# Optimization experiments

Measured on AMD Instinct MI355X. Metric: run time of the kernel, lower is better.

Reference implementation:

```python
import jax, jax.numpy as jnp
import numpy as np

B, T, IMG, PS, D, DEPTH, NH = 1, 8, 224, 16, 768, 12, 12
HP = IMG // PS
NP = HP * HP          # 196 patches per frame
N = NP + 1            # +1 cls token per frame
DH = D // NH
MLP = 4 * D
SCALE = DH ** -0.5


def _ln(x, g, b):
    mu = x.mean(-1, keepdims=True)
    var = ((x - mu) ** 2).mean(-1, keepdims=True)
    return (x - mu) / jnp.sqrt(var + 1e-5) * g + b


def _forward(x, W_patch, b_patch, cls_token, pos_embed,
             ln1_g, ln1_b, qkv_w, qkv_b, proj_w, proj_b,
             ln2_g, ln2_b, fc1_w, fc1_b, fc2_w, fc2_b, lnf_g, lnf_b):
    Bc = x.shape[0]
    # --- patch embed (Conv3d k=(1,ps,ps), stride=(1,ps,ps) == per-frame patch matmul) ---
    p = x.reshape(Bc, T, 3, HP, PS, HP, PS).transpose(0, 1, 3, 5, 2, 4, 6)
    p = p.reshape(Bc, T, NP, 3 * PS * PS)
    emb = p @ W_patch.T + b_patch                     # [B,T,NP,D] (correct layout)
    # replicate torch flatten(3)/transpose(1,2)/reshape axis scramble:
    emb = jnp.swapaxes(emb, 2, 3).reshape(Bc, T, NP, D)
    cls = jnp.broadcast_to(cls_token.reshape(1, 1, 1, D), (Bc, T, 1, D))
    h = jnp.concatenate([cls, emb], axis=2) + pos_embed.reshape(1, 1, N, D)
    h = h.reshape(Bc, T * N, D)

    for i in range(DEPTH):
        # --- attention ---
        a = _ln(h, ln1_g[i], ln1_b[i])
        qkv = (a @ qkv_w[i] + qkv_b[i]).reshape(Bc, T * N, 3, NH, DH)
        q, k, v = (jnp.transpose(qkv[:, :, j], (0, 2, 1, 3)) for j in range(3))  # [B,H,S,dh]
        if i % 2 == 0:  # divided space-time
            qf = q.reshape(Bc, NH, T, N, DH)
            kf = k.reshape(Bc, NH, T, N, DH)
            vf = v.reshape(Bc, NH, T, N, DH)
            q_t = qf.mean(3, keepdims=True)           # [B,H,T,1,dh]
            k_t = kf.mean(3, keepdims=True)
            v_t = vf.mean(3, keepdims=True)
            attn_t = jax.nn.softmax(jnp.einsum('bhtqd,bhtkd->bhtqk', q_t, k_t) * SCALE, -1)
            x_t = jnp.einsum('bhtqk,bhtkd->bhtqd', attn_t, v_t)[:, :, :, 0]  # [B,H,T,dh]
            attn_s = jax.nn.softmax(jnp.einsum('bhtqd,bhtkd->bhtqk', qf, kf) * SCALE, -1)
            x_s = jnp.einsum('bhtqk,bhtkd->bhtqd', attn_s, vf)               # [B,H,T,N,dh]
            o = (x_s + x_t[:, :, :, None, :]).reshape(Bc, NH, T * N, DH)
        else:  # joint space-time
            attn = jax.nn.softmax(jnp.einsum('bhqd,bhkd->bhqk', q, k) * SCALE, -1)
            o = jnp.einsum('bhqk,bhkd->bhqd', attn, v)
        o = jnp.transpose(o, (0, 2, 1, 3)).reshape(Bc, T * N, D)
        h = h + (o @ proj_w[i] + proj_b[i])
        # --- mlp ---
        m = _ln(h, ln2_g[i], ln2_b[i])
        m = jax.nn.gelu(m @ fc1_w[i] + fc1_b[i], approximate=False)
        h = h + (m @ fc2_w[i] + fc2_b[i])

    return _ln(h, lnf_g, lnf_b).reshape(Bc, T, N, D)


def setup_inputs() -> dict:
    key = jax.random.key(0)
    ks = jax.random.split(key, 12)
    s = 0.02
    return {
        'x': jax.random.normal(ks[0], (B, T, 3, IMG, IMG), jnp.float32),
        'W_patch': jax.random.normal(ks[1], (D, 3 * PS * PS), jnp.float32) * s,
        'b_patch': jnp.zeros((D,), jnp.float32),
        'cls_token': jax.random.normal(ks[2], (1, 1, D), jnp.float32) * s,
        'pos_embed': jax.random.normal(ks[3], (1, N, D), jnp.float32) * s,
        'ln1_g': jnp.ones((DEPTH, D), jnp.float32),
        'ln1_b': jnp.zeros((DEPTH, D), jnp.float32),
        'qkv_w': jax.random.normal(ks[4], (DEPTH, D, 3 * D), jnp.float32) * s,
        'qkv_b': jnp.zeros((DEPTH, 3 * D), jnp.float32),
        'proj_w': jax.random.normal(ks[5], (DEPTH, D, D), jnp.float32) * s,
        'proj_b': jnp.zeros((DEPTH, D), jnp.float32),
        'ln2_g': jnp.ones((DEPTH, D), jnp.float32),
        'ln2_b': jnp.zeros((DEPTH, D), jnp.float32),
        'fc1_w': jax.random.normal(ks[6], (DEPTH, D, MLP), jnp.float32) * s,
        'fc1_b': jnp.zeros((DEPTH, MLP), jnp.float32),
        'fc2_w': jax.random.normal(ks[7], (DEPTH, MLP, D), jnp.float32) * s,
        'fc2_b': jnp.zeros((DEPTH, D), jnp.float32),
        'lnf_g': jnp.ones((D,), jnp.float32),
        'lnf_b': jnp.zeros((D,), jnp.float32),
    }


def reference(x, W_patch, b_patch, cls_token, pos_embed,
              ln1_g, ln1_b, qkv_w, qkv_b, proj_w, proj_b,
              ln2_g, ln2_b, fc1_w, fc1_b, fc2_w, fc2_b, lnf_g, lnf_b):
    return _forward(x, W_patch, b_patch, cls_token, pos_embed,
                    ln1_g, ln1_b, qkv_w, qkv_b, proj_w, proj_b,
                    ln2_g, ln2_b, fc1_w, fc1_b, fc2_w, fc2_b, lnf_g, lnf_b)
```

## Files before the change

### kernel.cpp

```cpp
#include <hip/hip_runtime.h>
#include <math.h>

#define Dm 768
#define Tn 8
#define Nn 197
#define Sn 1576
#define MLPn 3072
#define NPn 196
#define MPAD 1664

typedef unsigned short u16;
typedef __bf16 bf16x8 __attribute__((ext_vector_type(8)));
typedef float f32x4 __attribute__((ext_vector_type(4)));
typedef unsigned int u32x4 __attribute__((ext_vector_type(4)));
typedef u16 u16x8 __attribute__((ext_vector_type(8)));
typedef u16 u16x4 __attribute__((ext_vector_type(4)));

__device__ inline u16 f2bf(float f) {
    union { float f; unsigned u; } v; v.f = f;
    unsigned r = v.u + 0x7fffu + ((v.u >> 16) & 1u);
    return (u16)(r >> 16);
}
__device__ inline float bf2f(u16 v) {
    union { unsigned u; float f; } x; x.u = ((unsigned)v) << 16; return x.f;
}

__device__ __forceinline__ void gl_lds16(const u16* __restrict__ g, u16* l) {
    __builtin_amdgcn_global_load_lds((const __attribute__((address_space(1))) void*)g,
                                     (__attribute__((address_space(3))) void*)l,
                                     16, 0, 0);
}

__global__ __launch_bounds__(256) void im2col_k(const float* __restrict__ x, u16* __restrict__ P) {
    int idx = blockIdx.x * 256 + threadIdx.x;
    if (idx >= 1568 * 768) return;
    int c = idx % 768, r = idx / 768;
    int p = r % 196, t = r / 196;
    int hp = p / 14, wp = p % 14;
    int ch = c / 256, rem = c % 256, py = rem / 16, px = rem % 16;
    P[idx] = f2bf(x[((t * 3 + ch) * 224 + hp * 16 + py) * 224 + wp * 16 + px]);
}

__global__ __launch_bounds__(256) void cvt_k(const float* __restrict__ s, u16* __restrict__ d, int n) {
    int i = blockIdx.x * 256 + threadIdx.x;
    if (i < n) d[i] = f2bf(s[i]);
}

__global__ __launch_bounds__(256) void cvtT_layer_k(const float* __restrict__ qw, const float* __restrict__ pw,
                                                    const float* __restrict__ f1w, const float* __restrict__ f2w,
                                                    u16* __restrict__ Wq, u16* __restrict__ Wp,
                                                    u16* __restrict__ W1, u16* __restrict__ W2) {
    __shared__ float tile[32][33];
    int bid = blockIdx.x;
    const float* src; u16* dst; int K, N, k0, n0;
    if (bid < 1728)      { src = qw;  dst = Wq; K = 768;  N = 2304; int r = bid;        k0 = (r / 72) * 32; n0 = (r % 72) * 32; }
    else if (bid < 2304) { src = pw;  dst = Wp; K = 768;  N = 768;  int r = bid - 1728; k0 = (r / 24) * 32; n0 = (r % 24) * 32; }
    else if (bid < 4608) { src = f1w; dst = W1; K = 768;  N = 3072; int r = bid - 2304; k0 = (r / 96) * 32; n0 = (r % 96) * 32; }
    else                 { src = f2w; dst = W2; K = 3072; N = 768;  int r = bid - 4608; k0 = (r / 24) * 32; n0 = (r % 24) * 32; }
    int tx = threadIdx.x & 31, ty = threadIdx.x >> 5;
#pragma unroll
    for (int i = 0; i < 4; ++i) tile[ty + 8 * i][tx] = src[(size_t)(k0 + ty + 8 * i) * N + n0 + tx];
    __syncthreads();
#pragma unroll
    for (int i = 0; i < 4; ++i) dst[(size_t)(n0 + ty + 8 * i) * K + k0 + tx] = f2bf(tile[tx][ty + 8 * i]);
}

__global__ __launch_bounds__(256) void build_h_k(const float* __restrict__ emb, const float* __restrict__ cls,
                                                 const float* __restrict__ pos, float* __restrict__ h) {
    int idx = blockIdx.x * 256 + threadIdx.x;
    if (idx >= Sn * Dm) return;
    int d = idx % Dm, s = idx / Dm;
    int t = s / Nn, r = s % Nn;
    float v;
    if (r == 0) v = cls[d];
    else {
        int f = (r - 1) * Dm + d;
        int p = f % NPn, dd = f / NPn;
        v = emb[(size_t)(t * NPn + p) * Dm + dd];
    }
    h[idx] = v + pos[r * Dm + d];
}

template <typename OutT>
__global__ __launch_bounds__(256) void ln_k(const float* __restrict__ X, const float* __restrict__ g,
                                            const float* __restrict__ bta, OutT* __restrict__ Y) {
    int row = blockIdx.x;
    const float* x = X + (size_t)row * Dm;
    float s = 0.f, s2 = 0.f;
#pragma unroll
    for (int q = 0; q < 3; ++q) {
        float v = x[threadIdx.x + q * 256];
        s += v; s2 += v * v;
    }
#pragma unroll
    for (int off = 1; off < 64; off <<= 1) {
        s  += __shfl_xor(s,  off);
        s2 += __shfl_xor(s2, off);
    }
    __shared__ float red[8];
    int wv = threadIdx.x >> 6;
    if ((threadIdx.x & 63) == 0) { red[wv * 2] = s; red[wv * 2 + 1] = s2; }
    __syncthreads();
    s  = red[0] + red[2] + red[4] + red[6];
    s2 = red[1] + red[3] + red[5] + red[7];
    float mu  = s * (1.f / 768.f);
    float var = s2 * (1.f / 768.f) - mu * mu;
    float rstd = rsqrtf(var + 1e-5f);
#pragma unroll
    for (int q = 0; q < 3; ++q) {
        int i = threadIdx.x + q * 256;
        float v = (x[i] - mu) * rstd * g[i] + bta[i];
        if constexpr (sizeof(OutT) == 2) Y[(size_t)row * Dm + i] = f2bf(v);
        else                             Y[(size_t)row * Dm + i] = v;
    }
}

__global__ __launch_bounds__(256) void mgemm_k(const u16* __restrict__ A, const u16* __restrict__ Bt,
                                               float* __restrict__ Cp, int N, int Kfull, int Kc) {
    __shared__ __align__(16) u16 As[4096];
    __shared__ __align__(16) u16 Bs[4096];
    int split = blockIdx.z;
    A  += split * Kc;
    Bt += split * Kc;
    Cp += (size_t)split * MPAD * N;
    int tid = threadIdx.x;
    int lane = tid & 63, w = tid >> 6;
    int wm = w & 1, wn = w >> 1;
    int m0 = blockIdx.y * 128, n0 = blockIdx.x * 128;
    f32x4 acc[4][4] = {};
    int c0 = tid, c1 = tid + 256;
    int ar0 = ((c0 >> 6) << 4) + (c0 & 15), ac0 = ((c0 >> 4) & 3) << 3;
    int ar1 = ((c1 >> 6) << 4) + (c1 & 15), ac1 = ((c1 >> 4) & 3) << 3;
    const u16* Arow0 = A  + (size_t)(m0 + ar0) * Kfull + ac0;
    const u16* Arow1 = A  + (size_t)(m0 + ar1) * Kfull + ac1;
    const u16* Brow0 = Bt + (size_t)(n0 + ar0) * Kfull + ac0;
    const u16* Brow1 = Bt + (size_t)(n0 + ar1) * Kfull + ac1;
    u16* As0 = As + (w * 64) * 8;
    u16* As1 = As + (256 + w * 64) * 8;
    u16* Bs0 = Bs + (w * 64) * 8;
    u16* Bs1 = Bs + (256 + w * 64) * 8;
    for (int k0 = 0; k0 < Kc; k0 += 32) {
        gl_lds16(Arow0 + k0, As0);
        gl_lds16(Arow1 + k0, As1);
        gl_lds16(Brow0 + k0, Bs0);
        gl_lds16(Brow1 + k0, Bs1);
        __syncthreads();
        bf16x8 af[4], bfr[4];
#pragma unroll
        for (int i = 0; i < 4; ++i) {
            af[i]  = *(const bf16x8*)(As + (((wm * 4 + i) * 64 + lane) << 3));
            bfr[i] = *(const bf16x8*)(Bs + (((wn * 4 + i) * 64 + lane) << 3));
        }
#pragma unroll
        for (int mi = 0; mi < 4; ++mi)
#pragma unroll
            for (int ni = 0; ni < 4; ++ni)
                acc[mi][ni] = __builtin_amdgcn_mfma_f32_16x16x32_bf16(af[mi], bfr[ni], acc[mi][ni], 0, 0, 0);
        __syncthreads();
    }
    int rbase = (lane >> 4) << 2, cl = lane & 15;
#pragma unroll
    for (int mi = 0; mi < 4; ++mi)
#pragma unroll
        for (int r = 0; r < 4; ++r) {
            int gm = m0 + wm * 64 + mi * 16 + rbase + r;
#pragma unroll
            for (int ni = 0; ni < 4; ++ni) {
                int gn = n0 + wn * 64 + ni * 16 + cl;
                Cp[(size_t)gm * N + gn] = acc[mi][ni][r];
            }
        }
}

template <bool GELU_ACT>
__global__ __launch_bounds__(256) void mgemm_fused_k(const u16* __restrict__ A, const u16* __restrict__ Bt,
                                                     const float* __restrict__ bias, u16* __restrict__ out,
                                                     int N, int Kfull, int Mout) {
    __shared__ __align__(16) u16 As[64 * 32];
    __shared__ __align__(16) u16 Bs[128 * 32];
    int tid = threadIdx.x;
    int lane = tid & 63, w = tid >> 6;
    int wm = w & 1, wn = w >> 1;
    int m0 = blockIdx.y * 64, n0 = blockIdx.x * 128;
    f32x4 acc[2][4] = {};
    int ca = tid;
    int ar = ((ca >> 6) << 4) + (ca & 15), ac = ((ca >> 4) & 3) << 3;
    const u16* Arow = A + (size_t)(m0 + ar) * Kfull + ac;
    int cb1 = tid + 256;
    int br1 = ((cb1 >> 6) << 4) + (cb1 & 15), bc1 = ((cb1 >> 4) & 3) << 3;
    const u16* Brow0 = Bt + (size_t)(n0 + ar) * Kfull + ac;
    const u16* Brow1 = Bt + (size_t)(n0 + br1) * Kfull + bc1;
    u16* Asw  = As + (w * 64) * 8;
    u16* Bsw0 = Bs + (w * 64) * 8;
    u16* Bsw1 = Bs + (256 + w * 64) * 8;
    for (int k0 = 0; k0 < Kfull; k0 += 32) {
        gl_lds16(Arow + k0, Asw);
        gl_lds16(Brow0 + k0, Bsw0);
        gl_lds16(Brow1 + k0, Bsw1);
        __syncthreads();
        bf16x8 af[2], bfr[4];
#pragma unroll
        for (int i = 0; i < 2; ++i) af[i]  = *(const bf16x8*)(As + (((wm * 2 + i) * 64 + lane) << 3));
#pragma unroll
        for (int j = 0; j < 4; ++j) bfr[j] = *(const bf16x8*)(Bs + (((wn * 4 + j) * 64 + lane) << 3));
#pragma unroll
        for (int mi = 0; mi < 2; ++mi)
#pragma unroll
            for (int ni = 0; ni < 4; ++ni)
                acc[mi][ni] = __builtin_amdgcn_mfma_f32_16x16x32_bf16(af[mi], bfr[ni], acc[mi][ni], 0, 0, 0);
        __syncthreads();
    }
    int rbase = (lane >> 4) << 2, cl = lane & 15;
#pragma unroll
    for (int mi = 0; mi < 2; ++mi)
#pragma unroll
        for (int r = 0; r < 4; ++r) {
            int gm = m0 + wm * 32 + mi * 16 + rbase + r;
            if (gm < Mout) {
#pragma unroll
                for (int ni = 0; ni < 4; ++ni) {
                    int gn = n0 + wn * 64 + ni * 16 + cl;
                    float v = acc[mi][ni][r] + bias[gn];
                    if (GELU_ACT) v = 0.5f * v * (1.f + erff(v * 0.7071067811865476f));
                    out[(size_t)gm * N + gn] = f2bf(v);
                }
            }
        }
}

__global__ __launch_bounds__(256) void ep_k(const float* __restrict__ Cp, const float* __restrict__ bias,
                                            float* __restrict__ out, int N, int S) {
    int row = blockIdx.y;
    int n = blockIdx.x * 1024 + threadIdx.x * 4;
    if (n >= N) return;
    size_t off = (size_t)row * N + n;
    f32x4 acc = *(const f32x4*)(Cp + off);
    for (int s = 1; s < S; ++s)
        acc += *(const f32x4*)(Cp + (size_t)s * MPAD * N + off);
    acc += *(const f32x4*)(bias + n);
    *(f32x4*)(out + off) = acc;
}

template <bool FINALOUT>
__global__ __launch_bounds__(256) void ep_ln_k(const float* __restrict__ Cp, const float* __restrict__ bias,
                                               float* __restrict__ h, const float* __restrict__ g,
                                               const float* __restrict__ bta, void* __restrict__ lnout, int S) {
    int row = blockIdx.x;
    int t = threadIdx.x;
    float v[3];
    float s = 0.f, s2 = 0.f;
#pragma unroll
    for (int q = 0; q < 3; ++q) {
        int i = t + q * 256;
        size_t off = (size_t)row * Dm + i;
        float a = Cp[off];
        for (int sp = 1; sp < S; ++sp) a += Cp[(size_t)sp * MPAD * Dm + off];
        a += bias[i] + h[off];
        h[off] = a;
        v[q] = a; s += a; s2 += a * a;
    }
#pragma unroll
    for (int off = 1; off < 64; off <<= 1) {
        s  += __shfl_xor(s,  off);
        s2 += __shfl_xor(s2, off);
    }
    __shared__ float red[8];
    int wv = t >> 6;
    if ((t & 63) == 0) { red[wv * 2] = s; red[wv * 2 + 1] = s2; }
    __syncthreads();
    s  = red[0] + red[2] + red[4] + red[6];
    s2 = red[1] + red[3] + red[5] + red[7];
    float mu  = s * (1.f / 768.f);
    float var = s2 * (1.f / 768.f) - mu * mu;
    float rstd = rsqrtf(var + 1e-5f);
#pragma unroll
    for (int q = 0; q < 3; ++q) {
        int i = t + q * 256;
        float y = (v[q] - mu) * rstd * g[i] + bta[i];
        if constexpr (FINALOUT) ((float*)lnout)[(size_t)row * Dm + i] = y;
        else                    ((u16*)lnout)[(size_t)row * Dm + i] = f2bf(y);
    }
}

__global__ __launch_bounds__(64) void vmean_k(const u16* __restrict__ qkv, float* __restrict__ vm) {
    int g = blockIdx.x;
    int h = g >> 3, t = g & 7;
    int d = threadIdx.x;
    float s = 0.f;
    for (int n = 0; n < Nn; ++n)
        s += bf2f(qkv[(size_t)(t * Nn + n) * 2304 + 1536 + h * 64 + d]);
    vm[g * 64 + d] = s * (1.f / 197.f);
}

__global__ __launch_bounds__(256) void attn_mfma_k(const u16* __restrict__ qkv, float* __restrict__ Ou,
                                                   float* __restrict__ ml, int even, int nsplit,
                                                   int NG, int Sq) {
    __shared__ __align__(16) u16 Ks[64 * 64];
    __shared__ __align__(16) u16 Vt[64 * 64];
    __shared__ __align__(16) u16 Ps[4 * 32 * 64];
    int g = blockIdx.y;
    int h, sbase;
    if (even) { h = g >> 3; sbase = (g & 7) * Nn; } else { h = g; sbase = 0; }
    int split = blockIdx.z;
    int chunk = (Sq + nsplit - 1) / nsplit;
    int kbeg = split * chunk, kend = min(Sq, kbeg + chunk);
    int tid = threadIdx.x, lane = tid & 63, w = tid >> 6;
    int quad = lane >> 4, l15 = lane & 15;
    int q0w = blockIdx.x * 128 + w * 32;
    u16* Pw = Ps + w * 2048;

    bf16x8 aq[2][2];
#pragma unroll
    for (int mb = 0; mb < 2; ++mb) {
        int qidx = q0w + mb * 16 + l15; if (qidx >= Sq) qidx = Sq - 1;
        const u16* qp = qkv + (size_t)(sbase + qidx) * 2304 + h * 64;
#pragma unroll
        for (int ks = 0; ks < 2; ++ks)
            aq[mb][ks] = *(const bf16x8*)(qp + ks * 32 + quad * 8);
    }
    f32x4 acc_o[2][4] = {};
    float m_run[2][4], l_run[2][4];
#pragma unroll
    for (int mb = 0; mb < 2; ++mb)
#pragma unroll
        for (int r = 0; r < 4; ++r) { m_run[mb][r] = -INFINITY; l_run[mb][r] = 0.f; }

    for (int kt = kbeg; kt < kend; kt += 64) {
        int cnt = kend - kt; if (cnt > 64) cnt = 64;
        {
            int dc = tid & 7;
#pragma unroll
            for (int p = 0; p < 2; ++p) {
                int row = (tid >> 3) + 32 * p;
                u32x4 kd = {};
                if (row < cnt) kd = *(const u32x4*)(qkv + (size_t)(sbase + kt + row) * 2304 + 768 + h * 64 + dc * 8);
                *(u32x4*)(Ks + row * 64 + ((dc ^ (row & 7)) << 3)) = kd;
            }
        }
        {
            int d = (tid & 31) * 2, kc = tid >> 5;
            u16x8 lo, hi;
#pragma unroll
            for (int i = 0; i < 8; ++i) {
                int key = kc * 8 + i;
                unsigned t = 0;
                if (key < cnt) t = *(const unsigned*)(qkv + (size_t)(sbase + kt + key) * 2304 + 1536 + h * 64 + d);
                lo[i] = (u16)(t & 0xffffu); hi[i] = (u16)(t >> 16);
            }
            *(u16x8*)(Vt + d * 64 + ((kc ^ (d & 7)) << 3)) = lo;
            *(u16x8*)(Vt + (d + 1) * 64 + ((kc ^ ((d + 1) & 7)) << 3)) = hi;
        }
        __syncthreads();
        f32x4 acc_s[2][4] = {};
#pragma unroll
        for (int ni = 0; ni < 4; ++ni) {
            int key = l15 + ni * 16;
#pragma unroll
            for (int ks = 0; ks < 2; ++ks) {
                bf16x8 bk = *(const bf16x8*)(Ks + key * 64 + ((((ks << 2) + quad) ^ (key & 7)) << 3));
                acc_s[0][ni] = __builtin_amdgcn_mfma_f32_16x16x32_bf16(aq[0][ks], bk, acc_s[0][ni], 0, 0, 0);
                acc_s[1][ni] = __builtin_amdgcn_mfma_f32_16x16x32_bf16(aq[1][ks], bk, acc_s[1][ni], 0, 0, 0);
            }
        }
#pragma unroll
        for (int mb = 0; mb < 2; ++mb) {
#pragma unroll
            for (int ni = 0; ni < 4; ++ni) {
                int keyabs = kt + l15 + ni * 16;
#pragma unroll
                for (int r = 0; r < 4; ++r) {
                    float sv = acc_s[mb][ni][r] * 0.125f;
                    if (keyabs >= kend) sv = -1e30f;
                    acc_s[mb][ni][r] = sv;
                }
            }
#pragma unroll
            for (int r = 0; r < 4; ++r) {
                float mx = fmaxf(fmaxf(acc_s[mb][0][r], acc_s[mb][1][r]), fmaxf(acc_s[mb][2][r], acc_s[mb][3][r]));
                mx = fmaxf(mx, __shfl_xor(mx, 1));
                mx = fmaxf(mx, __shfl_xor(mx, 2));
                mx = fmaxf(mx, __shfl_xor(mx, 4));
                mx = fmaxf(mx, __shfl_xor(mx, 8));
                float mnew = fmaxf(m_run[mb][r], mx);
                float pv[4], ps = 0.f;
#pragma unroll
                for (int ni = 0; ni < 4; ++ni) { pv[ni] = __expf(acc_s[mb][ni][r] - mnew); ps += pv[ni]; }
                ps += __shfl_xor(ps, 1);
                ps += __shfl_xor(ps, 2);
                ps += __shfl_xor(ps, 4);
                ps += __shfl_xor(ps, 8);
                float alpha = __expf(m_run[mb][r] - mnew);
                l_run[mb][r] = l_run[mb][r] * alpha + ps;
                m_run[mb][r] = mnew;
#pragma unroll
                for (int ni = 0; ni < 4; ++ni) acc_o[mb][ni][r] *= alpha;
                int prow = mb * 16 + quad * 4 + r;
#pragma unroll
                for (int ni = 0; ni < 4; ++ni) {
                    int key = l15 + ni * 16;
                    Pw[prow * 64 + (((key >> 3) ^ (prow & 7)) << 3) + (key & 7)] = f2bf(pv[ni]);
                }
            }
        }
        bf16x8 ap[2][2];
#pragma unroll
        for (int mb = 0; mb < 2; ++mb)
#pragma unroll
            for (int ks = 0; ks < 2; ++ks)
                ap[mb][ks] = *(const bf16x8*)(Pw + (mb * 16 + l15) * 64 + ((((ks << 2) + quad) ^ (l15 & 7)) << 3));
#pragma unroll
        for (int ni = 0; ni < 4; ++ni) {
            int d = l15 + ni * 16;
#pragma unroll
            for (int ks = 0; ks < 2; ++ks) {
                bf16x8 bv = *(const bf16x8*)(Vt + d * 64 + ((((ks << 2) + quad) ^ (d & 7)) << 3));
                acc_o[0][ni] = __builtin_amdgcn_mfma_f32_16x16x32_bf16(ap[0][ks], bv, acc_o[0][ni], 0, 0, 0);
                acc_o[1][ni] = __builtin_amdgcn_mfma_f32_16x16x32_bf16(ap[1][ks], bv, acc_o[1][ni], 0, 0, 0);
            }
        }
        __syncthreads();
    }
    size_t gb = ((size_t)split * NG + g) * Sq;
#pragma unroll
    for (int mb = 0; mb < 2; ++mb)
#pragma unroll
        for (int r = 0; r < 4; ++r) {
            int q = q0w + mb * 16 + quad * 4 + r;
            if (q < Sq) {
                float* op = Ou + (gb + q) * 64;
#pragma unroll
                for (int ni = 0; ni < 4; ++ni) op[l15 + ni * 16] = acc_o[mb][ni][r];
                if (l15 == 0) {
                    ml[(gb + q) * 2]     = m_run[mb][r];
                    ml[(gb + q) * 2 + 1] = l_run[mb][r];
                }
            }
        }
}

__global__ __launch_bounds__(256) void comb_k(const float* __restrict__ Ou, const float* __restrict__ ml,
                                              const float* __restrict__ vm, u16* __restrict__ ob,
                                              int even, int nsplit, int NG, int Sq) {
    int g = blockIdx.y;
    int q = blockIdx.x * 4 + (threadIdx.x >> 6);
    int d = threadIdx.x & 63;
    if (q >= Sq) return;
    int h, sbase;
    if (even) { h = g >> 3; sbase = (g & 7) * Nn; } else { h = g; sbase = 0; }
    float M = -INFINITY;
    for (int s = 0; s < nsplit; ++s) M = fmaxf(M, ml[(((size_t)s * NG + g) * Sq + q) * 2]);
    float num = 0.f, den = 0.f;
    for (int s = 0; s < nsplit; ++s) {
        size_t base = ((size_t)s * NG + g) * Sq + q;
        float wgt = __expf(ml[base * 2] - M);
        den += wgt * ml[base * 2 + 1];
        num += wgt * Ou[base * 64 + d];
    }
    float o = num / den;
    if (even) o += vm[g * 64 + d];
    ob[(size_t)(sbase + q) * Dm + h * 64 + d] = f2bf(o);
}

extern "C" void kernel_launch(void* const* d_in, const int* in_sizes, int n_in,
                              void* d_out, int out_size, void* d_ws, size_t ws_size,
                              hipStream_t stream) {
    (void)in_sizes; (void)n_in; (void)out_size; (void)ws_size;
    const float* x       = (const float*)d_in[0];
    const float* W_patch = (const float*)d_in[1];
    const float* b_patch = (const float*)d_in[2];
    const float* cls     = (const float*)d_in[3];
    const float* pos     = (const float*)d_in[4];
    const float* ln1_g   = (const float*)d_in[5];
    const float* ln1_b   = (const float*)d_in[6];
    const float* qkv_w   = (const float*)d_in[7];
    const float* qkv_b   = (const float*)d_in[8];
    const float* proj_w  = (const float*)d_in[9];
    const float* proj_b  = (const float*)d_in[10];
    const float* ln2_g   = (const float*)d_in[11];
    const float* ln2_b   = (const float*)d_in[12];
    const float* fc1_w   = (const float*)d_in[13];
    const float* fc1_b   = (const float*)d_in[14];
    const float* fc2_w   = (const float*)d_in[15];
    const float* fc2_b   = (const float*)d_in[16];
    const float* lnf_g   = (const float*)d_in[17];
    const float* lnf_b   = (const float*)d_in[18];

    char* base = (char*)d_ws;
    auto alloc = [&](size_t bytes) { void* p = base; base += (bytes + 255) & ~(size_t)255; return p; };
    u16*   P    = (u16*)  alloc((size_t)MPAD * 768 * 2);
    u16*   Wq   = (u16*)  alloc((size_t)2304 * 768 * 2);
    u16*   Wp   = (u16*)  alloc((size_t)768 * 768 * 2);
    u16*   W1   = (u16*)  alloc((size_t)3072 * 768 * 2);
    u16*   W2   = (u16*)  alloc((size_t)768 * 3072 * 2);
    float* emb  = (float*)alloc((size_t)1568 * 768 * 4);
    float* h    = (float*)alloc((size_t)Sn * Dm * 4);
    u16*   a    = (u16*)  alloc((size_t)MPAD * 768 * 2);
    u16*   qkvb = (u16*)  alloc((size_t)Sn * 2304 * 2);
    u16*   ob   = (u16*)  alloc((size_t)MPAD * 768 * 2);
    u16*   mb   = (u16*)  alloc((size_t)MPAD * 3072 * 2);
    float* vm   = (float*)alloc((size_t)96 * 64 * 4);
    float* Ou   = (float*)alloc((size_t)3 * 12 * Sn * 64 * 4);
    float* ml   = (float*)alloc((size_t)3 * 12 * Sn * 2 * 4);
    float* Cp   = (float*)alloc((size_t)4 * MPAD * 768 * 4);

    im2col_k<<<(1568 * 768 + 255) / 256, 256, 0, stream>>>(x, P);
    cvt_k<<<(768 * 768 + 255) / 256, 256, 0, stream>>>(W_patch, Wp, 768 * 768);
    mgemm_k<<<dim3(6, 13, 3), 256, 0, stream>>>(P, Wp, Cp, 768, 768, 256);
    ep_k<<<dim3(1, 1568), 256, 0, stream>>>(Cp, b_patch, emb, 768, 3);
    build_h_k<<<(Sn * Dm + 255) / 256, 256, 0, stream>>>(emb, cls, pos, h);
    ln_k<u16><<<Sn, 256, 0, stream>>>(h, ln1_g, ln1_b, a);

    for (int i = 0; i < 12; ++i) {
        cvtT_layer_k<<<6912, 256, 0, stream>>>(
            qkv_w + (size_t)i * 768 * 2304, proj_w + (size_t)i * 768 * 768,
            fc1_w + (size_t)i * 768 * 3072, fc2_w + (size_t)i * 3072 * 768,
            Wq, Wp, W1, W2);
        mgemm_fused_k<false><<<dim3(18, 26), 256, 0, stream>>>(a, Wq, qkv_b + i * 2304, qkvb, 2304, 768, Sn);
        if ((i & 1) == 0) {
            vmean_k<<<96, 64, 0, stream>>>(qkvb, vm);
            attn_mfma_k<<<dim3(2, 96, 1), 256, 0, stream>>>(qkvb, Ou, ml, 1, 1, 96, Nn);
            comb_k<<<dim3(50, 96), 256, 0, stream>>>(Ou, ml, vm, ob, 1, 1, 96, Nn);
        } else {
            attn_mfma_k<<<dim3(13, 12, 3), 256, 0, stream>>>(qkvb, Ou, ml, 0, 3, 12, Sn);
            comb_k<<<dim3(394, 12), 256, 0, stream>>>(Ou, ml, vm, ob, 0, 3, 12, Sn);
        }
        mgemm_k<<<dim3(6, 13, 4), 256, 0, stream>>>(ob, Wp, Cp, 768, 768, 192);
        ep_ln_k<false><<<Sn, 256, 0, stream>>>(Cp, proj_b + i * Dm, h, ln2_g + i * Dm, ln2_b + i * Dm, a, 4);
        mgemm_fused_k<true><<<dim3(24, 26), 256, 0, stream>>>(a, W1, fc1_b + i * MLPn, mb, 3072, 768, Sn);
        mgemm_k<<<dim3(6, 13, 4), 256, 0, stream>>>(mb, W2, Cp, 768, 3072, 768);
        if (i < 11)
            ep_ln_k<false><<<Sn, 256, 0, stream>>>(Cp, fc2_b + i * Dm, h, ln1_g + (i + 1) * Dm, ln1_b + (i + 1) * Dm, a, 4);
        else
            ep_ln_k<true><<<Sn, 256, 0, stream>>>(Cp, fc2_b + i * Dm, h, lnf_g, lnf_b, d_out, 4);
    }
}
```

Measured before the change: 2.369 ms.

## Double-buffer GEMM LDS tiles, fuse divided-attention normalization, parallelize v-mean

Both MFMA GEMM kernels now double-buffer their LDS tiles, issuing the global-to-LDS loads for the next K step before computing on the current one, with one barrier per iteration instead of two. For divided (even) layers the attention kernel normalizes its output and adds the temporal v-mean itself, so the combine kernel launch and the Ou/ml round trip are dropped. vmean_k uses 256 threads with a shared-memory reduction instead of 64. LDS use per GEMM block doubles, which may lower occupancy.

```diff
diff --git a/kernel.cpp b/kernel.cpp
--- a/kernel.cpp
+++ b/kernel.cpp
@@ -117,8 +117,8 @@
 
 __global__ __launch_bounds__(256) void mgemm_k(const u16* __restrict__ A, const u16* __restrict__ Bt,
                                                float* __restrict__ Cp, int N, int Kfull, int Kc) {
-    __shared__ __align__(16) u16 As[4096];
-    __shared__ __align__(16) u16 Bs[4096];
+    __shared__ __align__(16) u16 As[2 * 4096];
+    __shared__ __align__(16) u16 Bs[2 * 4096];
     int split = blockIdx.z;
     A  += split * Kc;
     Bt += split * Kc;
@@ -135,28 +135,35 @@
     const u16* Arow1 = A  + (size_t)(m0 + ar1) * Kfull + ac1;
     const u16* Brow0 = Bt + (size_t)(n0 + ar0) * Kfull + ac0;
     const u16* Brow1 = Bt + (size_t)(n0 + ar1) * Kfull + ac1;
-    u16* As0 = As + (w * 64) * 8;
-    u16* As1 = As + (256 + w * 64) * 8;
-    u16* Bs0 = Bs + (w * 64) * 8;
-    u16* Bs1 = Bs + (256 + w * 64) * 8;
+    auto STAGE = [&](int buf, int k0) {
+        int bo = buf << 12;
+        gl_lds16(Arow0 + k0, As + bo + (w * 64) * 8);
+        gl_lds16(Arow1 + k0, As + bo + (256 + w * 64) * 8);
+        gl_lds16(Brow0 + k0, Bs + bo + (w * 64) * 8);
+        gl_lds16(Brow1 + k0, Bs + bo + (256 + w * 64) * 8);
+    };
+    STAGE(0, 0);
+    asm volatile("s_waitcnt vmcnt(0)" ::: "memory");
+    __builtin_amdgcn_s_barrier();
+    int cur = 0;
     for (int k0 = 0; k0 < Kc; k0 += 32) {
-        gl_lds16(Arow0 + k0, As0);
-        gl_lds16(Arow1 + k0, As1);
-        gl_lds16(Brow0 + k0, Bs0);
-        gl_lds16(Brow1 + k0, Bs1);
-        __syncthreads();
+        if (k0 + 32 < Kc) STAGE(cur ^ 1, k0 + 32);
+        const u16* Ab = As + (cur << 12);
+        const u16* Bb = Bs + (cur << 12);
         bf16x8 af[4], bfr[4];
 #pragma unroll
         for (int i = 0; i < 4; ++i) {
-            af[i]  = *(const bf16x8*)(As + (((wm * 4 + i) * 64 + lane) << 3));
-            bfr[i] = *(const bf16x8*)(Bs + (((wn * 4 + i) * 64 + lane) << 3));
+            af[i]  = *(const bf16x8*)(Ab + (((wm * 4 + i) * 64 + lane) << 3));
+            bfr[i] = *(const bf16x8*)(Bb + (((wn * 4 + i) * 64 + lane) << 3));
         }
 #pragma unroll
         for (int mi = 0; mi < 4; ++mi)
 #pragma unroll
             for (int ni = 0; ni < 4; ++ni)
                 acc[mi][ni] = __builtin_amdgcn_mfma_f32_16x16x32_bf16(af[mi], bfr[ni], acc[mi][ni], 0, 0, 0);
-        __syncthreads();
+        asm volatile("s_waitcnt vmcnt(0)" ::: "memory");
+        __builtin_amdgcn_s_barrier();
+        cur ^= 1;
     }
     int rbase = (lane >> 4) << 2, cl = lane & 15;
 #pragma unroll
@@ -176,8 +183,8 @@
 __global__ __launch_bounds__(256) void mgemm_fused_k(const u16* __restrict__ A, const u16* __restrict__ Bt,
                                                      const float* __restrict__ bias, u16* __restrict__ out,
                                                      int N, int Kfull, int Mout) {
-    __shared__ __align__(16) u16 As[64 * 32];
-    __shared__ __align__(16) u16 Bs[128 * 32];
+    __shared__ __align__(16) u16 As[2 * 64 * 32];
+    __shared__ __align__(16) u16 Bs[2 * 128 * 32];
     int tid = threadIdx.x;
     int lane = tid & 63, w = tid >> 6;
     int wm = w & 1, wn = w >> 1;
@@ -190,25 +197,32 @@
     int br1 = ((cb1 >> 6) << 4) + (cb1 & 15), bc1 = ((cb1 >> 4) & 3) << 3;
     const u16* Brow0 = Bt + (size_t)(n0 + ar) * Kfull + ac;
     const u16* Brow1 = Bt + (size_t)(n0 + br1) * Kfull + bc1;
-    u16* Asw  = As + (w * 64) * 8;
-    u16* Bsw0 = Bs + (w * 64) * 8;
-    u16* Bsw1 = Bs + (256 + w * 64) * 8;
+    auto STAGE = [&](int buf, int k0) {
+        gl_lds16(Arow + k0, As + (buf << 11) + (w * 64) * 8);
+        gl_lds16(Brow0 + k0, Bs + (buf << 12) + (w * 64) * 8);
+        gl_lds16(Brow1 + k0, Bs + (buf << 12) + (256 + w * 64) * 8);
+    };
+    STAGE(0, 0);
+    asm volatile("s_waitcnt vmcnt(0)" ::: "memory");
+    __builtin_amdgcn_s_barrier();
+    int cur = 0;
     for (int k0 = 0; k0 < Kfull; k0 += 32) {
-        gl_lds16(Arow + k0, Asw);
-        gl_lds16(Brow0 + k0, Bsw0);
-        gl_lds16(Brow1 + k0, Bsw1);
-        __syncthreads();
+        if (k0 + 32 < Kfull) STAGE(cur ^ 1, k0 + 32);
+        const u16* Ab = As + (cur << 11);
+        const u16* Bb = Bs + (cur << 12);
         bf16x8 af[2], bfr[4];
 #pragma unroll
-        for (int i = 0; i < 2; ++i) af[i]  = *(const bf16x8*)(As + (((wm * 2 + i) * 64 + lane) << 3));
-#pragma unroll
-        for (int j = 0; j < 4; ++j) bfr[j] = *(const bf16x8*)(Bs + (((wn * 4 + j) * 64 + lane) << 3));
+        for (int i = 0; i < 2; ++i) af[i]  = *(const bf16x8*)(Ab + (((wm * 2 + i) * 64 + lane) << 3));
+#pragma unroll
+        for (int j = 0; j < 4; ++j) bfr[j] = *(const bf16x8*)(Bb + (((wn * 4 + j) * 64 + lane) << 3));
 #pragma unroll
         for (int mi = 0; mi < 2; ++mi)
 #pragma unroll
             for (int ni = 0; ni < 4; ++ni)
                 acc[mi][ni] = __builtin_amdgcn_mfma_f32_16x16x32_bf16(af[mi], bfr[ni], acc[mi][ni], 0, 0, 0);
-        __syncthreads();
+        asm volatile("s_waitcnt vmcnt(0)" ::: "memory");
+        __builtin_amdgcn_s_barrier();
+        cur ^= 1;
     }
     int rbase = (lane >> 4) << 2, cl = lane & 15;
 #pragma unroll
@@ -282,19 +296,23 @@
     }
 }
 
-__global__ __launch_bounds__(64) void vmean_k(const u16* __restrict__ qkv, float* __restrict__ vm) {
+__global__ __launch_bounds__(256) void vmean_k(const u16* __restrict__ qkv, float* __restrict__ vm) {
     int g = blockIdx.x;
     int h = g >> 3, t = g & 7;
-    int d = threadIdx.x;
+    int d = threadIdx.x & 63, part = threadIdx.x >> 6;
     float s = 0.f;
-    for (int n = 0; n < Nn; ++n)
+    for (int n = part; n < Nn; n += 4)
         s += bf2f(qkv[(size_t)(t * Nn + n) * 2304 + 1536 + h * 64 + d]);
-    vm[g * 64 + d] = s * (1.f / 197.f);
+    __shared__ float red[256];
+    red[threadIdx.x] = s;
+    __syncthreads();
+    if (part == 0) vm[g * 64 + d] = (red[d] + red[64 + d] + red[128 + d] + red[192 + d]) * (1.f / 197.f);
 }
 
 __global__ __launch_bounds__(256) void attn_mfma_k(const u16* __restrict__ qkv, float* __restrict__ Ou,
-                                                   float* __restrict__ ml, int even, int nsplit,
-                                                   int NG, int Sq) {
+                                                   float* __restrict__ ml, const float* __restrict__ vm,
+                                                   u16* __restrict__ ob, int even, int nsplit,
+                                                   int NG, int Sq, int fuse) {
     __shared__ __align__(16) u16 Ks[64 * 64];
     __shared__ __align__(16) u16 Vt[64 * 64];
     __shared__ __align__(16) u16 Ps[4 * 32 * 64];
@@ -420,33 +438,49 @@
         }
         __syncthreads();
     }
-    size_t gb = ((size_t)split * NG + g) * Sq;
-#pragma unroll
-    for (int mb = 0; mb < 2; ++mb)
-#pragma unroll
-        for (int r = 0; r < 4; ++r) {
-            int q = q0w + mb * 16 + quad * 4 + r;
-            if (q < Sq) {
-                float* op = Ou + (gb + q) * 64;
-#pragma unroll
-                for (int ni = 0; ni < 4; ++ni) op[l15 + ni * 16] = acc_o[mb][ni][r];
-                if (l15 == 0) {
-                    ml[(gb + q) * 2]     = m_run[mb][r];
-                    ml[(gb + q) * 2 + 1] = l_run[mb][r];
+    if (fuse) {
+#pragma unroll
+        for (int mb = 0; mb < 2; ++mb)
+#pragma unroll
+            for (int r = 0; r < 4; ++r) {
+                int q = q0w + mb * 16 + quad * 4 + r;
+                if (q < Sq) {
+                    float inv = 1.f / l_run[mb][r];
+                    u16* op = ob + (size_t)(sbase + q) * Dm + h * 64;
+#pragma unroll
+                    for (int ni = 0; ni < 4; ++ni) {
+                        int d = l15 + ni * 16;
+                        op[d] = f2bf(acc_o[mb][ni][r] * inv + vm[g * 64 + d]);
+                    }
                 }
             }
-        }
+    } else {
+        size_t gb = ((size_t)split * NG + g) * Sq;
+#pragma unroll
+        for (int mb = 0; mb < 2; ++mb)
+#pragma unroll
+            for (int r = 0; r < 4; ++r) {
+                int q = q0w + mb * 16 + quad * 4 + r;
+                if (q < Sq) {
+                    float* op = Ou + (gb + q) * 64;
+#pragma unroll
+                    for (int ni = 0; ni < 4; ++ni) op[l15 + ni * 16] = acc_o[mb][ni][r];
+                    if (l15 == 0) {
+                        ml[(gb + q) * 2]     = m_run[mb][r];
+                        ml[(gb + q) * 2 + 1] = l_run[mb][r];
+                    }
+                }
+            }
+    }
 }
 
 __global__ __launch_bounds__(256) void comb_k(const float* __restrict__ Ou, const float* __restrict__ ml,
-                                              const float* __restrict__ vm, u16* __restrict__ ob,
-                                              int even, int nsplit, int NG, int Sq) {
+                                              u16* __restrict__ ob, int nsplit, int NG, int Sq) {
     int g = blockIdx.y;
     int q = blockIdx.x * 4 + (threadIdx.x >> 6);
     int d = threadIdx.x & 63;
     if (q >= Sq) return;
-    int h, sbase;
-    if (even) { h = g >> 3; sbase = (g & 7) * Nn; } else { h = g; sbase = 0; }
+    int h = g, sbase = 0;
     float M = -INFINITY;
     for (int s = 0; s < nsplit; ++s) M = fmaxf(M, ml[(((size_t)s * NG + g) * Sq + q) * 2]);
     float num = 0.f, den = 0.f;
@@ -457,7 +491,6 @@
         num += wgt * Ou[base * 64 + d];
     }
     float o = num / den;
-    if (even) o += vm[g * 64 + d];
     ob[(size_t)(sbase + q) * Dm + h * 64 + d] = f2bf(o);
 }
 
@@ -517,12 +550,11 @@
             Wq, Wp, W1, W2);
         mgemm_fused_k<false><<<dim3(18, 26), 256, 0, stream>>>(a, Wq, qkv_b + i * 2304, qkvb, 2304, 768, Sn);
         if ((i & 1) == 0) {
-            vmean_k<<<96, 64, 0, stream>>>(qkvb, vm);
-            attn_mfma_k<<<dim3(2, 96, 1), 256, 0, stream>>>(qkvb, Ou, ml, 1, 1, 96, Nn);
-            comb_k<<<dim3(50, 96), 256, 0, stream>>>(Ou, ml, vm, ob, 1, 1, 96, Nn);
+            vmean_k<<<96, 256, 0, stream>>>(qkvb, vm);
+            attn_mfma_k<<<dim3(2, 96, 1), 256, 0, stream>>>(qkvb, Ou, ml, vm, ob, 1, 1, 96, Nn, 1);
         } else {
-            attn_mfma_k<<<dim3(13, 12, 3), 256, 0, stream>>>(qkvb, Ou, ml, 0, 3, 12, Sn);
-            comb_k<<<dim3(394, 12), 256, 0, stream>>>(Ou, ml, vm, ob, 0, 3, 12, Sn);
+            attn_mfma_k<<<dim3(13, 12, 3), 256, 0, stream>>>(qkvb, Ou, ml, vm, ob, 0, 3, 12, Sn, 0);
+            comb_k<<<dim3(394, 12), 256, 0, stream>>>(Ou, ml, ob, 3, 12, Sn);
         }
         mgemm_k<<<dim3(6, 13, 4), 256, 0, stream>>>(ob, Wp, Cp, 768, 768, 192);
         ep_ln_k<false><<<Sn, 256, 0, stream>>>(Cp, proj_b + i * Dm, h, ln2_g + i * Dm, ln2_b + i * Dm, a, 4);
```

Result: faster. 2.279 ms (-3.8%).
